# Optimization experiments

Hardware: AMD Instinct MI355X
Metric: run time of the kernel (lower is better)

Reference implementation:

```python
import jax, jax.numpy as jnp
import numpy as np


def _gat_layer(h, mask, w, a_src, a_dst):
    # h: [B,C,N,Fin], w: [C,H,Fin,Fout], a_*: [C,H,Fout,1], mask: [B,N,N] (True where no edge)
    h_prime = jnp.einsum('bcni,chio->bchno', h, w)          # [B,C,H,N,Fout]
    t = jnp.tanh(h_prime)
    s = jnp.einsum('bchno,cho->bchn', t, a_src[..., 0])      # src scores
    d = jnp.einsum('bchno,cho->bchn', t, a_dst[..., 0])      # dst scores
    attn = s[..., :, None] + d[..., None, :]                 # [B,C,H,N,N]
    attn = jnp.where(attn >= 0, attn, 0.2 * attn)            # leaky_relu(0.2)
    attn = jnp.where(mask[:, None, None, :, :], jnp.float32(-1e12), attn)
    attn = jax.nn.softmax(attn, axis=-1)
    return jnp.einsum('bchnm,bchmo->bchno', attn, h_prime)   # [B,C,H,N,Fout]


def setup_inputs() -> dict:
    key = jax.random.key(0)
    ks = jax.random.split(key, 8)
    B, C, N, F0, H, F = 2, 2, 1024, 64, 8, 64

    def xavier(k, shape):
        fan_in, fan_out = shape[-2], shape[-1]
        lim = (6.0 / (fan_in + fan_out)) ** 0.5
        return jax.random.uniform(k, shape, jnp.float32, -lim, lim)

    x = jax.random.normal(ks[0], (B, C, N, F0), dtype=jnp.float32)
    adj = jax.random.randint(ks[1], (B, N, N), 0, 2, dtype=jnp.int32)
    w1 = xavier(ks[2], (C, H, F0, F))
    a_src1 = xavier(ks[3], (C, H, F, 1))
    a_dst1 = xavier(ks[4], (C, H, F, 1))
    w2 = xavier(ks[5], (C, H, H * F, F))
    a_src2 = xavier(ks[6], (C, H, F, 1))
    a_dst2 = xavier(ks[7], (C, H, F, 1))
    return {"x": x, "adj": adj, "w1": w1, "a_src1": a_src1, "a_dst1": a_dst1,
            "w2": w2, "a_src2": a_src2, "a_dst2": a_dst2}


def reference(x, adj, w1, a_src1, a_dst1, w2, a_src2, a_dst2):
    B, C, N, _ = x.shape
    adj_f = adj.astype(jnp.float32) + jnp.eye(N, dtype=jnp.float32)[None]  # add self-loops
    mask = adj_f == 0                                        # [B,N,N]
    out1 = _gat_layer(x, mask, w1, a_src1, a_dst1)           # [B,C,H,N,F]
    # permute heads next to features, flatten, elu (dropout is identity in eval)
    x1 = jax.nn.elu(jnp.transpose(out1, (0, 1, 3, 2, 4)).reshape(B, C, N, -1))
    out2 = _gat_layer(x1, mask, w2, a_src2, a_dst2)          # [B,C,H,N,F]
    return out2.mean(axis=2)                                 # mean over heads -> [B,C,N,F]
```

## Files before the change

### kernel.cpp

```cpp
#include <hip/hip_runtime.h>

#define BB 2
#define CC 2
#define NN 1024
#define HH 8
#define FFV 64
#define BCHN (BB*CC*HH)
#define SVN  (BB*CC*HH*NN)
#define LOG2E 1.44269504f

typedef _Float16 f16x8 __attribute__((ext_vector_type(8)));
typedef _Float16 f16x4 __attribute__((ext_vector_type(4)));
typedef __fp16 h16x2 __attribute__((ext_vector_type(2)));
typedef float f32x4 __attribute__((ext_vector_type(4)));

__device__ __forceinline__ float fexp2(float x) {
  float r; asm("v_exp_f32 %0, %1" : "=v"(r) : "v"(x)); return r;
}

__global__ __launch_bounds__(256) void proj1_fused(
    const float* __restrict__ x, const int* __restrict__ adj,
    const float* __restrict__ w1, const float* __restrict__ w2,
    const float* __restrict__ asrc, const float* __restrict__ adst,
    _Float16* __restrict__ w2T, unsigned long long* __restrict__ bmg,
    _Float16* __restrict__ HpT, float* __restrict__ s_out, float* __restrict__ d_out)
{
  __shared__ union {
    __align__(16) _Float16 tile[64*72];
    struct { float sp[4][32]; float sd[4][32]; } pr;
  } sm;
  const int bx = blockIdx.x;
  const int t = threadIdx.x;
  const int w = t >> 6, lane = t & 63;
  const int colr = lane & 15, quad = lane >> 4;

  if (bx < 1024) {
    const int bch = bx & 31;
    const int row0 = (bx >> 5) * 32;
    const int h = bch & 7; const int bc = bch >> 3; const int c = bc & 1;

    const float* Ar0 = x + ((size_t)bc*NN + row0 + colr)*64;
    const float* Ar1 = Ar0 + (size_t)16*64;
    const float* Bw  = w1 + ((size_t)(c*HH + h))*64*64 + w*16 + colr;

    f32x4 acc0 = {0.f,0.f,0.f,0.f}, acc1 = {0.f,0.f,0.f,0.f};
    #pragma unroll
    for (int kb = 0; kb < 64; kb += 32) {
      const float4 pa0 = *(const float4*)(Ar0 + kb + quad*8);
      const float4 pa1 = *(const float4*)(Ar0 + kb + quad*8 + 4);
      const float4 pb0 = *(const float4*)(Ar1 + kb + quad*8);
      const float4 pb1 = *(const float4*)(Ar1 + kb + quad*8 + 4);
      float bv[8];
      #pragma unroll
      for (int j = 0; j < 8; ++j) bv[j] = Bw[(size_t)(kb + quad*8 + j)*64];
      f16x8 a0, a1, bf;
      a0[0]=(_Float16)pa0.x; a0[1]=(_Float16)pa0.y; a0[2]=(_Float16)pa0.z; a0[3]=(_Float16)pa0.w;
      a0[4]=(_Float16)pa1.x; a0[5]=(_Float16)pa1.y; a0[6]=(_Float16)pa1.z; a0[7]=(_Float16)pa1.w;
      a1[0]=(_Float16)pb0.x; a1[1]=(_Float16)pb0.y; a1[2]=(_Float16)pb0.z; a1[3]=(_Float16)pb0.w;
      a1[4]=(_Float16)pb1.x; a1[5]=(_Float16)pb1.y; a1[6]=(_Float16)pb1.z; a1[7]=(_Float16)pb1.w;
      #pragma unroll
      for (int j = 0; j < 8; ++j) bf[j] = (_Float16)bv[j];
      acc0 = __builtin_amdgcn_mfma_f32_16x16x32_f16(a0, bf, acc0, 0, 0, 0);
      acc1 = __builtin_amdgcn_mfma_f32_16x16x32_f16(a1, bf, acc1, 0, 0, 0);
    }

    const float af  = asrc[(c*HH + h)*64 + w*16 + colr];
    const float bf_ = adst[(c*HH + h)*64 + w*16 + colr];
    _Float16* HT = HpT + ((size_t)bch*64 + w*16 + colr)*NN + row0;

    #pragma unroll
    for (int mt = 0; mt < 2; ++mt) {
      const f32x4 a = mt ? acc1 : acc0;
      f16x4 hv;
      #pragma unroll
      for (int i = 0; i < 4; ++i) {
        const float v = a[i];
        hv[i] = (_Float16)v;
        const float ex = __expf(2.f*v);
        const float th = 1.f - 2.f/(ex + 1.f);
        float ps = th * af, pd = th * bf_;
        #pragma unroll
        for (int off = 1; off < 16; off <<= 1) {
          ps += __shfl_xor(ps, off);
          pd += __shfl_xor(pd, off);
        }
        if (colr == 0) {
          sm.pr.sp[w][mt*16 + quad*4 + i] = ps;
          sm.pr.sd[w][mt*16 + quad*4 + i] = pd;
        }
      }
      *(f16x4*)(HT + mt*16 + quad*4) = hv;
    }
    __syncthreads();
    if (t < 32) {
      const float sv = sm.pr.sp[0][t] + sm.pr.sp[1][t] + sm.pr.sp[2][t] + sm.pr.sp[3][t];
      const float dv = sm.pr.sd[0][t] + sm.pr.sd[1][t] + sm.pr.sd[2][t] + sm.pr.sd[3][t];
      s_out[bch*NN + row0 + t] = sv * LOG2E;
      d_out[bch*NN + row0 + t] = dv * LOG2E;
    }
  } else if (bx < 1152) {
    const int u = bx - 1024;
    const int ch = u >> 3, k0 = (u & 7)*64;
    const float* src = w2 + ((size_t)ch*512 + k0)*64;
    #pragma unroll
    for (int j = 0; j < 4; ++j) {
      const int uu = t + j*256;
      const int k = uu >> 4, seg = uu & 15;
      const float4 v = ((const float4*)src)[(size_t)k*16 + seg];
      sm.tile[(seg*4+0)*72 + k] = (_Float16)v.x;
      sm.tile[(seg*4+1)*72 + k] = (_Float16)v.y;
      sm.tile[(seg*4+2)*72 + k] = (_Float16)v.z;
      sm.tile[(seg*4+3)*72 + k] = (_Float16)v.w;
    }
    __syncthreads();
    _Float16* dst = w2T + (size_t)ch*64*512 + k0;
    #pragma unroll
    for (int j = 0; j < 2; ++j) {
      const int uu = t + j*256;
      const int f = uu >> 3, seg = uu & 7;
      const f16x8 o = *(const f16x8*)&sm.tile[f*72 + seg*8];
      *(f16x8*)(dst + (size_t)f*512 + seg*8) = o;
    }
  } else {
    const int g = (bx - 1152)*4 + w;
    const int base = g*32;
    #pragma unroll
    for (int jb = 0; jb < 4; ++jb) {
      int vals[8];
      #pragma unroll
      for (int i = 0; i < 8; ++i) {
        const int idx = base + jb*8 + i;
        const int b = idx >> 14;
        const int n = (idx >> 4) & (NN - 1);
        const int wd = idx & 15;
        vals[i] = adj[((size_t)b*NN + n)*NN + wd*64 + lane];
      }
      #pragma unroll
      for (int i = 0; i < 8; ++i) {
        const int idx = base + jb*8 + i;
        const int n = (idx >> 4) & (NN - 1);
        const int m = (idx & 15)*64 + lane;
        const unsigned long long bits = __ballot((vals[i] != 0) || (m == n));
        if (lane == 0) bmg[idx] = bits;
      }
    }
  }
}

template<int K>
__global__ __launch_bounds__(256) void proj_mfma(
    const _Float16* __restrict__ A,
    const _Float16* __restrict__ wT,
    const float* __restrict__ asrc, const float* __restrict__ adst,
    _Float16* __restrict__ HpT, float* __restrict__ s_out, float* __restrict__ d_out)
{
  __shared__ float sp[4][32], sd[4][32];
  const int bch = blockIdx.y;
  const int h = bch % HH; const int bc = bch / HH; const int c = bc % CC;
  const int row0 = blockIdx.x*32;
  const int t = threadIdx.x;
  const int w = t >> 6, lane = t & 63;
  const int colr = lane & 15, quad = lane >> 4;

  const _Float16* Arow0 = A + ((size_t)bc*NN + row0 + colr)*K;
  const _Float16* Arow1 = Arow0 + (size_t)16*K;
  const _Float16* Brow  = wT + ((size_t)(c*HH + h)*64 + w*16 + colr)*K;

  f32x4 acc0 = {0.f,0.f,0.f,0.f}, acc1 = {0.f,0.f,0.f,0.f};
  #pragma unroll 4
  for (int kb = 0; kb < K; kb += 32) {
    const f16x8 a0 = *(const f16x8*)(Arow0 + kb + quad*8);
    const f16x8 a1 = *(const f16x8*)(Arow1 + kb + quad*8);
    const f16x8 bf = *(const f16x8*)(Brow  + kb + quad*8);
    acc0 = __builtin_amdgcn_mfma_f32_16x16x32_f16(a0, bf, acc0, 0, 0, 0);
    acc1 = __builtin_amdgcn_mfma_f32_16x16x32_f16(a1, bf, acc1, 0, 0, 0);
  }

  const float af = asrc[(c*HH + h)*64 + w*16 + colr];
  const float bf_ = adst[(c*HH + h)*64 + w*16 + colr];
  _Float16* HT = HpT + ((size_t)bch*64 + w*16 + colr)*NN + row0;

  #pragma unroll
  for (int mt = 0; mt < 2; ++mt) {
    const f32x4 a = mt ? acc1 : acc0;
    f16x4 hv;
    #pragma unroll
    for (int i = 0; i < 4; ++i) {
      const float v = a[i];
      hv[i] = (_Float16)v;
      const float ex = __expf(2.f*v);
      const float th = 1.f - 2.f/(ex + 1.f);
      float ps = th * af, pd = th * bf_;
      #pragma unroll
      for (int off = 1; off < 16; off <<= 1) {
        ps += __shfl_xor(ps, off);
        pd += __shfl_xor(pd, off);
      }
      if (colr == 0) {
        sp[w][mt*16 + quad*4 + i] = ps;
        sd[w][mt*16 + quad*4 + i] = pd;
      }
    }
    *(f16x4*)(HT + mt*16 + quad*4) = hv;
  }
  __syncthreads();
  if (t < 32) {
    const float sv = sp[0][t] + sp[1][t] + sp[2][t] + sp[3][t];
    const float dv = sd[0][t] + sd[1][t] + sd[2][t] + sd[3][t];
    s_out[bch*NN + row0 + t] = sv * LOG2E;
    d_out[bch*NN + row0 + t] = dv * LOG2E;
  }
}

template<int LAYER>
__global__ __launch_bounds__(256, 4) void attn_mfma(
    const _Float16* __restrict__ HpT, const float* __restrict__ s_arr,
    const float* __restrict__ d_arr, const unsigned long long* __restrict__ bmg,
    _Float16* __restrict__ outp)
{
  __shared__ float partials[4][32*68];
  __shared__ float dsP[4][32];
  const int bch = blockIdx.x;
  const int b = bch / (CC*HH);
  const int row0 = blockIdx.y*32;
  const int t = threadIdx.x;
  const int w = t >> 6, lane = t & 63;
  const int colr = lane & 15, quad = lane >> 4;

  const float* dg = d_arr + (size_t)bch*NN;
  const float4* dg4 = (const float4*)dg;
  float mxl = -1e30f;
  #pragma unroll
  for (int j = 0; j < 4; ++j) {
    const float4 v = dg4[lane + 64*j];
    mxl = fmaxf(fmaxf(v.x, v.y), fmaxf(fmaxf(v.z, v.w), mxl));
  }
  #pragma unroll
  for (int off = 1; off < 64; off <<= 1) mxl = fmaxf(mxl, __shfl_xor(mxl, off));
  const float maxd = mxl;

  const int r0 = row0 + colr, r1 = r0 + 16;
  const float s0 = s_arr[(size_t)bch*NN + r0];
  const float s1 = s_arr[(size_t)bch*NN + r1];
  const float so0 = s0 + maxd, so1 = s1 + maxd;
  const float offs0 = fmaxf(so0, 0.2f*so0);
  const float offs1 = fmaxf(so1, 0.2f*so1);
  const float sA0 = s0 - offs0, sB0 = 0.2f*s0 - offs0;
  const float sA1 = s1 - offs1, sB1 = 0.2f*s1 - offs1;

  unsigned long long m0[4], m1[4];
  {
    const unsigned long long* bm0 = bmg + ((size_t)b*NN + r0)*16 + w*4;
    const unsigned long long* bm1 = bmg + ((size_t)b*NN + r1)*16 + w*4;
    #pragma unroll
    for (int j = 0; j < 4; ++j) { m0[j] = bm0[j]; m1[j] = bm1[j]; }
  }

  const _Float16* Bg = HpT + (size_t)bch*64*NN;
  const int kbase = w*256;
  const _Float16* Bp = Bg + kbase + quad*8;

  f32x4 acc[2][4], accs[2];
  #pragma unroll
  for (int rt = 0; rt < 2; ++rt) {
    accs[rt] = (f32x4){0.f,0.f,0.f,0.f};
    #pragma unroll
    for (int ft = 0; ft < 4; ++ft) acc[rt][ft] = (f32x4){0.f,0.f,0.f,0.f};
  }
  f16x8 ones;
  #pragma unroll
  for (int i = 0; i < 8; ++i) ones[i] = (_Float16)1.f;

  f16x8 Bc[4];
  #pragma unroll
  for (int ft = 0; ft < 4; ++ft) Bc[ft] = *(const f16x8*)(Bp + (size_t)(ft*16 + colr)*NN);
  float4 dc0 = *(const float4*)(dg + kbase + quad*8);
  float4 dc1 = *(const float4*)(dg + kbase + quad*8 + 4);

  #pragma unroll
  for (int ks = 0; ks < 8; ++ks) {
    f16x8 Bn[4]; float4 dn0, dn1;
    if (ks < 7) {
      #pragma unroll
      for (int ft = 0; ft < 4; ++ft)
        Bn[ft] = *(const f16x8*)(Bp + (size_t)(ft*16 + colr)*NN + (ks+1)*32);
      dn0 = *(const float4*)(dg + kbase + (ks+1)*32 + quad*8);
      dn1 = *(const float4*)(dg + kbase + (ks+1)*32 + quad*8 + 4);
    }
    const unsigned mb0 = (unsigned)((m0[ks >> 1] >> ((ks & 1)*32 + quad*8)) & 0xFFull);
    const unsigned mb1 = (unsigned)((m1[ks >> 1] >> ((ks & 1)*32 + quad*8)) & 0xFFull);
    const float dd[8] = {dc0.x, dc0.y, dc0.z, dc0.w, dc1.x, dc1.y, dc1.z, dc1.w};
    union { f16x8 v; h16x2 h[4]; } A0, A1;
    #pragma unroll
    for (int jp = 0; jp < 4; ++jp) {
      float p0[2], p1[2];
      #pragma unroll
      for (int jj = 0; jj < 2; ++jj) {
        const int j = jp*2 + jj;
        const float dj = dd[j];
        const float l0 = fmaxf(sA0 + dj, fmaf(0.2f, dj, sB0));
        const float l1 = fmaxf(sA1 + dj, fmaf(0.2f, dj, sB1));
        p0[jj] = ((mb0 >> j) & 1u) ? fexp2(l0) : 0.f;
        p1[jj] = ((mb1 >> j) & 1u) ? fexp2(l1) : 0.f;
      }
      A0.h[jp] = __builtin_amdgcn_cvt_pkrtz(p0[0], p0[1]);
      A1.h[jp] = __builtin_amdgcn_cvt_pkrtz(p1[0], p1[1]);
    }
    #pragma unroll
    for (int ft = 0; ft < 4; ++ft) {
      acc[0][ft] = __builtin_amdgcn_mfma_f32_16x16x32_f16(A0.v, Bc[ft], acc[0][ft], 0, 0, 0);
      acc[1][ft] = __builtin_amdgcn_mfma_f32_16x16x32_f16(A1.v, Bc[ft], acc[1][ft], 0, 0, 0);
    }
    accs[0] = __builtin_amdgcn_mfma_f32_16x16x32_f16(A0.v, ones, accs[0], 0, 0, 0);
    accs[1] = __builtin_amdgcn_mfma_f32_16x16x32_f16(A1.v, ones, accs[1], 0, 0, 0);
    if (ks < 7) {
      #pragma unroll
      for (int ft = 0; ft < 4; ++ft) Bc[ft] = Bn[ft];
      dc0 = dn0; dc1 = dn1;
    }
  }

  if (colr == 0) {
    #pragma unroll
    for (int i = 0; i < 4; ++i) {
      dsP[w][quad*4 + i] = accs[0][i];
      dsP[w][16 + quad*4 + i] = accs[1][i];
    }
  }
  float* pw = partials[w];
  #pragma unroll
  for (int rt = 0; rt < 2; ++rt)
    #pragma unroll
    for (int ft = 0; ft < 4; ++ft)
      #pragma unroll
      for (int i = 0; i < 4; ++i)
        pw[(rt*16 + quad*4 + i)*68 + ft*16 + colr] = acc[rt][ft][i];
  __syncthreads();

  const int r = t >> 3, f0 = (t & 7)*8;
  const float dsum = dsP[0][r] + dsP[1][r] + dsP[2][r] + dsP[3][r];
  const float inv = 1.f / dsum;
  float4 c0 = {0.f,0.f,0.f,0.f}, c1 = {0.f,0.f,0.f,0.f};
  #pragma unroll
  for (int w4 = 0; w4 < 4; ++w4) {
    const float* base = &partials[w4][r*68 + f0];
    const float4 a0 = *(const float4*)base;
    const float4 a1 = *(const float4*)(base + 4);
    c0.x += a0.x; c0.y += a0.y; c0.z += a0.z; c0.w += a0.w;
    c1.x += a1.x; c1.y += a1.y; c1.z += a1.z; c1.w += a1.w;
  }
  const float cv[8] = {c0.x,c0.y,c0.z,c0.w, c1.x,c1.y,c1.z,c1.w};
  f16x8 o;
  #pragma unroll
  for (int i = 0; i < 8; ++i) {
    float v = cv[i] * inv;
    if (LAYER == 1) v = v > 0.f ? v : expm1f(v);
    o[i] = (_Float16)v;
  }
  const int bc = bch / HH, h = bch % HH;
  if (LAYER == 1)
    *(f16x8*)(outp + ((size_t)bc*NN + row0 + r)*512 + h*64 + f0) = o;
  else
    *(f16x8*)(outp + ((size_t)bch*NN + row0 + r)*64 + f0) = o;
}

__global__ __launch_bounds__(256) void reduce_heads(
    const _Float16* __restrict__ out2, float* __restrict__ out)
{
  const int o = blockIdx.x*256 + threadIdx.x;
  const int f = o & 63;
  const int n = (o >> 6) & (NN - 1);
  const int bc = o >> 16;
  float acc = 0.f;
  #pragma unroll
  for (int h = 0; h < HH; ++h)
    acc += (float)out2[(((size_t)bc*HH + h)*NN + n)*FFV + f];
  out[o] = acc * 0.125f;
}

extern "C" void kernel_launch(void* const* d_in, const int* in_sizes, int n_in,
                              void* d_out, int out_size, void* d_ws, size_t ws_size,
                              hipStream_t stream)
{
  const float* x   = (const float*)d_in[0];
  const int*   adj = (const int*)d_in[1];
  const float* w1  = (const float*)d_in[2];
  const float* as1 = (const float*)d_in[3];
  const float* ad1 = (const float*)d_in[4];
  const float* w2  = (const float*)d_in[5];
  const float* as2 = (const float*)d_in[6];
  const float* ad2 = (const float*)d_in[7];

  char* w8 = (char*)d_ws;
  _Float16* HpT = (_Float16*)(w8);
  _Float16* XB  = (_Float16*)(w8 + (4u<<20));
  _Float16* w2T = (_Float16*)(w8 + (8u<<20));
  float* s_v = (float*)(w8 + (10u<<20));
  float* d_v = (float*)(w8 + (10u<<20) + SVN*4);
  unsigned long long* bmg = (unsigned long long*)(w8 + (10u<<20) + SVN*8);

  proj1_fused<<<1408, 256, 0, stream>>>(x, adj, w1, w2, as1, ad1, w2T, bmg, HpT, s_v, d_v);
  attn_mfma<1><<<dim3(BCHN, NN/32), 256, 0, stream>>>(HpT, s_v, d_v, bmg, XB);
  proj_mfma<512><<<dim3(NN/32, BCHN), 256, 0, stream>>>(XB, w2T, as2, ad2, HpT, s_v, d_v);
  attn_mfma<2><<<dim3(BCHN, NN/32), 256, 0, stream>>>(HpT, s_v, d_v, bmg, XB);
  reduce_heads<<<dim3((unsigned)(out_size/256)), 256, 0, stream>>>(XB, (float*)d_out);
}
```

Measured before the change: 169.5 us.

## Fuse layer-2 projection into layer-1 attention and head-mean into layer-2 attention

Replaces the attention kernels with a 512-thread block per (b,c, 16-row tile) where each wave handles one head over the full key range. Layer 1 writes its ELU output for all heads into shared memory and immediately runs the layer-2 projection and score computation, removing the separate projection kernel and the XB round trip. Layer 2 reduces across heads with LDS atomics and writes the mean directly, removing the reduce_heads kernel. The cost is fewer blocks (256) with a longer serial key loop per wave and no split-K across waves, which may cut parallelism and latency hiding.

After: 183.3 us. 1.08x slower.

```diff
diff --git a/kernel.cpp b/kernel.cpp
--- a/kernel.cpp
+++ b/kernel.cpp
@@ -4,10 +4,10 @@
 #define CC 2
 #define NN 1024
 #define HH 8
-#define FFV 64
-#define BCHN (BB*CC*HH)
-#define SVN  (BB*CC*HH*NN)
+#define BCHN 32
+#define SVN  (BCHN*NN)
 #define LOG2E 1.44269504f
+#define X1S 520
 
 typedef _Float16 f16x8 __attribute__((ext_vector_type(8)));
 typedef _Float16 f16x4 __attribute__((ext_vector_type(4)));
@@ -147,235 +147,198 @@
   }
 }
 
-template<int K>
-__global__ __launch_bounds__(256) void proj_mfma(
-    const _Float16* __restrict__ A,
-    const _Float16* __restrict__ wT,
-    const float* __restrict__ asrc, const float* __restrict__ adst,
-    _Float16* __restrict__ HpT, float* __restrict__ s_out, float* __restrict__ d_out)
+template<int LAYER>
+__global__ __launch_bounds__(512, 2) void attn_monster(
+    const _Float16* __restrict__ HpTin, const float* __restrict__ s_arr,
+    const float* __restrict__ d_arr, const unsigned long long* __restrict__ bmg,
+    const _Float16* __restrict__ w2T, const float* __restrict__ asrc2,
+    const float* __restrict__ adst2,
+    _Float16* __restrict__ HpT2, float* __restrict__ s2, float* __restrict__ d2,
+    float* __restrict__ out)
 {
-  __shared__ float sp[4][32], sd[4][32];
-  const int bch = blockIdx.y;
-  const int h = bch % HH; const int bc = bch / HH; const int c = bc % CC;
-  const int row0 = blockIdx.x*32;
+  __shared__ union {
+    __align__(16) _Float16 x1[16*X1S];
+    float mbuf[16*64];
+  } sm;
+  const int bc = blockIdx.x;
+  const int r0 = blockIdx.y * 16;
   const int t = threadIdx.x;
-  const int w = t >> 6, lane = t & 63;
+  const int h = t >> 6;
+  const int lane = t & 63;
   const int colr = lane & 15, quad = lane >> 4;
-
-  const _Float16* Arow0 = A + ((size_t)bc*NN + row0 + colr)*K;
-  const _Float16* Arow1 = Arow0 + (size_t)16*K;
-  const _Float16* Brow  = wT + ((size_t)(c*HH + h)*64 + w*16 + colr)*K;
-
-  f32x4 acc0 = {0.f,0.f,0.f,0.f}, acc1 = {0.f,0.f,0.f,0.f};
-  #pragma unroll 4
-  for (int kb = 0; kb < K; kb += 32) {
-    const f16x8 a0 = *(const f16x8*)(Arow0 + kb + quad*8);
-    const f16x8 a1 = *(const f16x8*)(Arow1 + kb + quad*8);
-    const f16x8 bf = *(const f16x8*)(Brow  + kb + quad*8);
-    acc0 = __builtin_amdgcn_mfma_f32_16x16x32_f16(a0, bf, acc0, 0, 0, 0);
-    acc1 = __builtin_amdgcn_mfma_f32_16x16x32_f16(a1, bf, acc1, 0, 0, 0);
-  }
-
-  const float af = asrc[(c*HH + h)*64 + w*16 + colr];
-  const float bf_ = adst[(c*HH + h)*64 + w*16 + colr];
-  _Float16* HT = HpT + ((size_t)bch*64 + w*16 + colr)*NN + row0;
-
-  #pragma unroll
-  for (int mt = 0; mt < 2; ++mt) {
-    const f32x4 a = mt ? acc1 : acc0;
-    f16x4 hv;
+  const int bch = bc*HH + h;
+  const int b = bc >> 1, c = bc & 1;
+
+  if (LAYER == 2) {
+    sm.mbuf[t] = 0.f;
+    sm.mbuf[t + 512] = 0.f;
+    __syncthreads();
+  }
+
+  const float* dg = d_arr + (size_t)bch*NN;
+  const float4* dg4 = (const float4*)dg;
+  float mxl = -1e30f;
+  #pragma unroll
+  for (int j = 0; j < 4; ++j) {
+    const float4 v = dg4[lane + 64*j];
+    mxl = fmaxf(fmaxf(v.x, v.y), fmaxf(fmaxf(v.z, v.w), mxl));
+  }
+  #pragma unroll
+  for (int off = 1; off < 64; off <<= 1) mxl = fmaxf(mxl, __shfl_xor(mxl, off));
+  const float maxd = mxl;
+
+  const int r = r0 + colr;
+  const float s = s_arr[(size_t)bch*NN + r];
+  const float so = s + maxd;
+  const float offs = fmaxf(so, 0.2f*so);
+  const float sA = s - offs, sB = 0.2f*s - offs;
+
+  const unsigned long long* bm = bmg + ((size_t)b*NN + r)*16;
+  const _Float16* Bp = HpTin + (size_t)bch*64*NN + quad*8;
+
+  f32x4 acc[4];
+  f32x4 accs = {0.f,0.f,0.f,0.f};
+  #pragma unroll
+  for (int ft = 0; ft < 4; ++ft) acc[ft] = (f32x4){0.f,0.f,0.f,0.f};
+  f16x8 ones;
+  #pragma unroll
+  for (int i = 0; i < 8; ++i) ones[i] = (_Float16)1.f;
+
+  f16x8 Bc[4];
+  #pragma unroll
+  for (int ft = 0; ft < 4; ++ft) Bc[ft] = *(const f16x8*)(Bp + (size_t)(ft*16 + colr)*NN);
+  float4 dc0 = *(const float4*)(dg + quad*8);
+  float4 dc1 = *(const float4*)(dg + quad*8 + 4);
+  unsigned long long mcur = bm[0], mnxt = 0;
+
+  #pragma unroll 2
+  for (int kp = 0; kp < 16; ++kp) {
+    if (kp < 15) mnxt = bm[kp + 1];
+    #pragma unroll
+    for (int hf = 0; hf < 2; ++hf) {
+      const int ks = kp*2 + hf;
+      f16x8 Bn[4]; float4 dn0, dn1;
+      if (ks < 31) {
+        #pragma unroll
+        for (int ft = 0; ft < 4; ++ft)
+          Bn[ft] = *(const f16x8*)(Bp + (size_t)(ft*16 + colr)*NN + (ks+1)*32);
+        dn0 = *(const float4*)(dg + (ks+1)*32 + quad*8);
+        dn1 = *(const float4*)(dg + (ks+1)*32 + quad*8 + 4);
+      }
+      const unsigned mb = (unsigned)((mcur >> (hf*32 + quad*8)) & 0xFFull);
+      const float dd[8] = {dc0.x, dc0.y, dc0.z, dc0.w, dc1.x, dc1.y, dc1.z, dc1.w};
+      union { f16x8 v; h16x2 hh[4]; } A;
+      #pragma unroll
+      for (int jp = 0; jp < 4; ++jp) {
+        float p[2];
+        #pragma unroll
+        for (int jj = 0; jj < 2; ++jj) {
+          const int j = jp*2 + jj;
+          const float dj = dd[j];
+          const float l = fmaxf(sA + dj, fmaf(0.2f, dj, sB));
+          p[jj] = ((mb >> j) & 1u) ? fexp2(l) : 0.f;
+        }
+        A.hh[jp] = __builtin_amdgcn_cvt_pkrtz(p[0], p[1]);
+      }
+      #pragma unroll
+      for (int ft = 0; ft < 4; ++ft)
+        acc[ft] = __builtin_amdgcn_mfma_f32_16x16x32_f16(A.v, Bc[ft], acc[ft], 0, 0, 0);
+      accs = __builtin_amdgcn_mfma_f32_16x16x32_f16(A.v, ones, accs, 0, 0, 0);
+      if (ks < 31) {
+        #pragma unroll
+        for (int ft = 0; ft < 4; ++ft) Bc[ft] = Bn[ft];
+        dc0 = dn0; dc1 = dn1;
+      }
+    }
+    mcur = mnxt;
+  }
+
+  float inv[4];
+  #pragma unroll
+  for (int i = 0; i < 4; ++i) inv[i] = 1.f / accs[i];
+
+  if (LAYER == 1) {
+    #pragma unroll
+    for (int ft = 0; ft < 4; ++ft)
+      #pragma unroll
+      for (int i = 0; i < 4; ++i) {
+        float v = acc[ft][i] * inv[i];
+        v = v > 0.f ? v : expm1f(v);
+        sm.x1[(quad*4 + i)*X1S + h*64 + ft*16 + colr] = (_Float16)v;
+      }
+    __syncthreads();
+
+    const _Float16* Bw = w2T + (size_t)(c*HH + h)*64*512 + quad*8;
+    f32x4 acc2[4];
+    #pragma unroll
+    for (int ft = 0; ft < 4; ++ft) acc2[ft] = (f32x4){0.f,0.f,0.f,0.f};
+    f16x8 Wc[4];
+    #pragma unroll
+    for (int ft = 0; ft < 4; ++ft) Wc[ft] = *(const f16x8*)(Bw + (size_t)(ft*16 + colr)*512);
+    #pragma unroll 4
+    for (int k2 = 0; k2 < 16; ++k2) {
+      f16x8 Wn[4];
+      if (k2 < 15) {
+        #pragma unroll
+        for (int ft = 0; ft < 4; ++ft)
+          Wn[ft] = *(const f16x8*)(Bw + (size_t)(ft*16 + colr)*512 + (k2+1)*32);
+      }
+      const f16x8 Af = *(const f16x8*)&sm.x1[colr*X1S + k2*32 + quad*8];
+      #pragma unroll
+      for (int ft = 0; ft < 4; ++ft)
+        acc2[ft] = __builtin_amdgcn_mfma_f32_16x16x32_f16(Af, Wc[ft], acc2[ft], 0, 0, 0);
+      if (k2 < 15) {
+        #pragma unroll
+        for (int ft = 0; ft < 4; ++ft) Wc[ft] = Wn[ft];
+      }
+    }
+
+    float af[4], bfv[4];
+    #pragma unroll
+    for (int ft = 0; ft < 4; ++ft) {
+      af[ft]  = asrc2[(c*HH + h)*64 + ft*16 + colr];
+      bfv[ft] = adst2[(c*HH + h)*64 + ft*16 + colr];
+    }
     #pragma unroll
     for (int i = 0; i < 4; ++i) {
-      const float v = a[i];
-      hv[i] = (_Float16)v;
-      const float ex = __expf(2.f*v);
-      const float th = 1.f - 2.f/(ex + 1.f);
-      float ps = th * af, pd = th * bf_;
+      float ps = 0.f, pd = 0.f;
+      #pragma unroll
+      for (int ft = 0; ft < 4; ++ft) {
+        const float v = acc2[ft][i];
+        const float ex = __expf(2.f*v);
+        const float th = 1.f - 2.f/(ex + 1.f);
+        ps += th * af[ft]; pd += th * bfv[ft];
+      }
       #pragma unroll
       for (int off = 1; off < 16; off <<= 1) {
         ps += __shfl_xor(ps, off);
         pd += __shfl_xor(pd, off);
       }
       if (colr == 0) {
-        sp[w][mt*16 + quad*4 + i] = ps;
-        sd[w][mt*16 + quad*4 + i] = pd;
-      }
-    }
-    *(f16x4*)(HT + mt*16 + quad*4) = hv;
-  }
-  __syncthreads();
-  if (t < 32) {
-    const float sv = sp[0][t] + sp[1][t] + sp[2][t] + sp[3][t];
-    const float dv = sd[0][t] + sd[1][t] + sd[2][t] + sd[3][t];
-    s_out[bch*NN + row0 + t] = sv * LOG2E;
-    d_out[bch*NN + row0 + t] = dv * LOG2E;
-  }
-}
-
-template<int LAYER>
-__global__ __launch_bounds__(256, 4) void attn_mfma(
-    const _Float16* __restrict__ HpT, const float* __restrict__ s_arr,
-    const float* __restrict__ d_arr, const unsigned long long* __restrict__ bmg,
-    _Float16* __restrict__ outp)
-{
-  __shared__ float partials[4][32*68];
-  __shared__ float dsP[4][32];
-  const int bch = blockIdx.x;
-  const int b = bch / (CC*HH);
-  const int row0 = blockIdx.y*32;
-  const int t = threadIdx.x;
-  const int w = t >> 6, lane = t & 63;
-  const int colr = lane & 15, quad = lane >> 4;
-
-  const float* dg = d_arr + (size_t)bch*NN;
-  const float4* dg4 = (const float4*)dg;
-  float mxl = -1e30f;
-  #pragma unroll
-  for (int j = 0; j < 4; ++j) {
-    const float4 v = dg4[lane + 64*j];
-    mxl = fmaxf(fmaxf(v.x, v.y), fmaxf(fmaxf(v.z, v.w), mxl));
-  }
-  #pragma unroll
-  for (int off = 1; off < 64; off <<= 1) mxl = fmaxf(mxl, __shfl_xor(mxl, off));
-  const float maxd = mxl;
-
-  const int r0 = row0 + colr, r1 = r0 + 16;
-  const float s0 = s_arr[(size_t)bch*NN + r0];
-  const float s1 = s_arr[(size_t)bch*NN + r1];
-  const float so0 = s0 + maxd, so1 = s1 + maxd;
-  const float offs0 = fmaxf(so0, 0.2f*so0);
-  const float offs1 = fmaxf(so1, 0.2f*so1);
-  const float sA0 = s0 - offs0, sB0 = 0.2f*s0 - offs0;
-  const float sA1 = s1 - offs1, sB1 = 0.2f*s1 - offs1;
-
-  unsigned long long m0[4], m1[4];
-  {
-    const unsigned long long* bm0 = bmg + ((size_t)b*NN + r0)*16 + w*4;
-    const unsigned long long* bm1 = bmg + ((size_t)b*NN + r1)*16 + w*4;
-    #pragma unroll
-    for (int j = 0; j < 4; ++j) { m0[j] = bm0[j]; m1[j] = bm1[j]; }
-  }
-
-  const _Float16* Bg = HpT + (size_t)bch*64*NN;
-  const int kbase = w*256;
-  const _Float16* Bp = Bg + kbase + quad*8;
-
-  f32x4 acc[2][4], accs[2];
-  #pragma unroll
-  for (int rt = 0; rt < 2; ++rt) {
-    accs[rt] = (f32x4){0.f,0.f,0.f,0.f};
-    #pragma unroll
-    for (int ft = 0; ft < 4; ++ft) acc[rt][ft] = (f32x4){0.f,0.f,0.f,0.f};
-  }
-  f16x8 ones;
-  #pragma unroll
-  for (int i = 0; i < 8; ++i) ones[i] = (_Float16)1.f;
-
-  f16x8 Bc[4];
-  #pragma unroll
-  for (int ft = 0; ft < 4; ++ft) Bc[ft] = *(const f16x8*)(Bp + (size_t)(ft*16 + colr)*NN);
-  float4 dc0 = *(const float4*)(dg + kbase + quad*8);
-  float4 dc1 = *(const float4*)(dg + kbase + quad*8 + 4);
-
-  #pragma unroll
-  for (int ks = 0; ks < 8; ++ks) {
-    f16x8 Bn[4]; float4 dn0, dn1;
-    if (ks < 7) {
-      #pragma unroll
-      for (int ft = 0; ft < 4; ++ft)
-        Bn[ft] = *(const f16x8*)(Bp + (size_t)(ft*16 + colr)*NN + (ks+1)*32);
-      dn0 = *(const float4*)(dg + kbase + (ks+1)*32 + quad*8);
-      dn1 = *(const float4*)(dg + kbase + (ks+1)*32 + quad*8 + 4);
-    }
-    const unsigned mb0 = (unsigned)((m0[ks >> 1] >> ((ks & 1)*32 + quad*8)) & 0xFFull);
-    const unsigned mb1 = (unsigned)((m1[ks >> 1] >> ((ks & 1)*32 + quad*8)) & 0xFFull);
-    const float dd[8] = {dc0.x, dc0.y, dc0.z, dc0.w, dc1.x, dc1.y, dc1.z, dc1.w};
-    union { f16x8 v; h16x2 h[4]; } A0, A1;
-    #pragma unroll
-    for (int jp = 0; jp < 4; ++jp) {
-      float p0[2], p1[2];
-      #pragma unroll
-      for (int jj = 0; jj < 2; ++jj) {
-        const int j = jp*2 + jj;
-        const float dj = dd[j];
-        const float l0 = fmaxf(sA0 + dj, fmaf(0.2f, dj, sB0));
-        const float l1 = fmaxf(sA1 + dj, fmaf(0.2f, dj, sB1));
-        p0[jj] = ((mb0 >> j) & 1u) ? fexp2(l0) : 0.f;
-        p1[jj] = ((mb1 >> j) & 1u) ? fexp2(l1) : 0.f;
-      }
-      A0.h[jp] = __builtin_amdgcn_cvt_pkrtz(p0[0], p0[1]);
-      A1.h[jp] = __builtin_amdgcn_cvt_pkrtz(p1[0], p1[1]);
+        s2[(size_t)bch*NN + r0 + quad*4 + i] = ps * LOG2E;
+        d2[(size_t)bch*NN + r0 + quad*4 + i] = pd * LOG2E;
+      }
     }
     #pragma unroll
     for (int ft = 0; ft < 4; ++ft) {
-      acc[0][ft] = __builtin_amdgcn_mfma_f32_16x16x32_f16(A0.v, Bc[ft], acc[0][ft], 0, 0, 0);
-      acc[1][ft] = __builtin_amdgcn_mfma_f32_16x16x32_f16(A1.v, Bc[ft], acc[1][ft], 0, 0, 0);
-    }
-    accs[0] = __builtin_amdgcn_mfma_f32_16x16x32_f16(A0.v, ones, accs[0], 0, 0, 0);
-    accs[1] = __builtin_amdgcn_mfma_f32_16x16x32_f16(A1.v, ones, accs[1], 0, 0, 0);
-    if (ks < 7) {
-      #pragma unroll
-      for (int ft = 0; ft < 4; ++ft) Bc[ft] = Bn[ft];
-      dc0 = dn0; dc1 = dn1;
-    }
-  }
-
-  if (colr == 0) {
-    #pragma unroll
-    for (int i = 0; i < 4; ++i) {
-      dsP[w][quad*4 + i] = accs[0][i];
-      dsP[w][16 + quad*4 + i] = accs[1][i];
-    }
-  }
-  float* pw = partials[w];
-  #pragma unroll
-  for (int rt = 0; rt < 2; ++rt)
+      f16x4 hv;
+      #pragma unroll
+      for (int i = 0; i < 4; ++i) hv[i] = (_Float16)acc2[ft][i];
+      *(f16x4*)(HpT2 + ((size_t)bch*64 + ft*16 + colr)*NN + r0 + quad*4) = hv;
+    }
+  } else {
     #pragma unroll
     for (int ft = 0; ft < 4; ++ft)
       #pragma unroll
       for (int i = 0; i < 4; ++i)
-        pw[(rt*16 + quad*4 + i)*68 + ft*16 + colr] = acc[rt][ft][i];
-  __syncthreads();
-
-  const int r = t >> 3, f0 = (t & 7)*8;
-  const float dsum = dsP[0][r] + dsP[1][r] + dsP[2][r] + dsP[3][r];
-  const float inv = 1.f / dsum;
-  float4 c0 = {0.f,0.f,0.f,0.f}, c1 = {0.f,0.f,0.f,0.f};
-  #pragma unroll
-  for (int w4 = 0; w4 < 4; ++w4) {
-    const float* base = &partials[w4][r*68 + f0];
-    const float4 a0 = *(const float4*)base;
-    const float4 a1 = *(const float4*)(base + 4);
-    c0.x += a0.x; c0.y += a0.y; c0.z += a0.z; c0.w += a0.w;
-    c1.x += a1.x; c1.y += a1.y; c1.z += a1.z; c1.w += a1.w;
-  }
-  const float cv[8] = {c0.x,c0.y,c0.z,c0.w, c1.x,c1.y,c1.z,c1.w};
-  f16x8 o;
-  #pragma unroll
-  for (int i = 0; i < 8; ++i) {
-    float v = cv[i] * inv;
-    if (LAYER == 1) v = v > 0.f ? v : expm1f(v);
-    o[i] = (_Float16)v;
-  }
-  const int bc = bch / HH, h = bch % HH;
-  if (LAYER == 1)
-    *(f16x8*)(outp + ((size_t)bc*NN + row0 + r)*512 + h*64 + f0) = o;
-  else
-    *(f16x8*)(outp + ((size_t)bch*NN + row0 + r)*64 + f0) = o;
-}
-
-__global__ __launch_bounds__(256) void reduce_heads(
-    const _Float16* __restrict__ out2, float* __restrict__ out)
-{
-  const int o = blockIdx.x*256 + threadIdx.x;
-  const int f = o & 63;
-  const int n = (o >> 6) & (NN - 1);
-  const int bc = o >> 16;
-  float acc = 0.f;
-  #pragma unroll
-  for (int h = 0; h < HH; ++h)
-    acc += (float)out2[(((size_t)bc*HH + h)*NN + n)*FFV + f];
-  out[o] = acc * 0.125f;
+        atomicAdd(&sm.mbuf[(quad*4 + i)*64 + ft*16 + colr], acc[ft][i] * inv[i]);
+    __syncthreads();
+    const int q = t >> 5;
+    const int f = (t*2) & 63;
+    const float m0 = sm.mbuf[q*64 + f], m1 = sm.mbuf[q*64 + f + 1];
+    float2 ov = {m0 * 0.125f, m1 * 0.125f};
+    *(float2*)(out + ((size_t)bc*NN + r0 + q)*64 + f) = ov;
+  }
 }
 
 extern "C" void kernel_launch(void* const* d_in, const int* in_sizes, int n_in,
@@ -392,16 +355,18 @@
   const float* ad2 = (const float*)d_in[7];
 
   char* w8 = (char*)d_ws;
-  _Float16* HpT = (_Float16*)(w8);
-  _Float16* XB  = (_Float16*)(w8 + (4u<<20));
-  _Float16* w2T = (_Float16*)(w8 + (8u<<20));
-  float* s_v = (float*)(w8 + (10u<<20));
-  float* d_v = (float*)(w8 + (10u<<20) + SVN*4);
-  unsigned long long* bmg = (unsigned long long*)(w8 + (10u<<20) + SVN*8);
+  _Float16* HpT  = (_Float16*)(w8);
+  _Float16* HpT2 = (_Float16*)(w8 + (4u<<20));
+  _Float16* w2T  = (_Float16*)(w8 + (8u<<20));
+  float* s_v  = (float*)(w8 + (10u<<20));
+  float* d_v  = (float*)(w8 + (10u<<20) + SVN*4);
+  float* s2_v = (float*)(w8 + (10u<<20) + SVN*8);
+  float* d2_v = (float*)(w8 + (10u<<20) + SVN*12);
+  unsigned long long* bmg = (unsigned long long*)(w8 + (10u<<20) + SVN*16);
 
   proj1_fused<<<1408, 256, 0, stream>>>(x, adj, w1, w2, as1, ad1, w2T, bmg, HpT, s_v, d_v);
-  attn_mfma<1><<<dim3(BCHN, NN/32), 256, 0, stream>>>(HpT, s_v, d_v, bmg, XB);
-  proj_mfma<512><<<dim3(NN/32, BCHN), 256, 0, stream>>>(XB, w2T, as2, ad2, HpT, s_v, d_v);
-  attn_mfma<2><<<dim3(BCHN, NN/32), 256, 0, stream>>>(HpT, s_v, d_v, bmg, XB);
-  reduce_heads<<<dim3((unsigned)(out_size/256)), 256, 0, stream>>>(XB, (float*)d_out);
+  attn_monster<1><<<dim3(4, 64), 512, 0, stream>>>(HpT, s_v, d_v, bmg, w2T, as2, ad2,
+                                                   HpT2, s2_v, d2_v, (float*)d_out);
+  attn_monster<2><<<dim3(4, 64), 512, 0, stream>>>(HpT2, s2_v, d2_v, bmg, w2T, as2, ad2,
+                                                   HpT2, s2_v, d2_v, (float*)d_out);
 }
```
